# Kernel tuning notes

Measured on AMD Instinct MI355X. Metric: run time of the kernel, lower is better.

## Reference

```python
import jax, jax.numpy as jnp
import numpy as np

BS, Q, NC, T = 8, 500, 2, 400


def setup_inputs() -> dict:
    key = jax.random.key(0)
    k1, k2, k3, k4, k5 = jax.random.split(key, 5)
    pred_logits = jax.random.normal(k1, (BS, Q, NC), dtype=jnp.float32)
    pred_keypoints = jax.random.normal(k2, (BS, Q, 53), dtype=jnp.float32)
    tgt_ids = jax.random.randint(k3, (T,), 0, NC)
    # target keypoints: [center(2) | offsets(34)] ~ N(0, .2), visibility(17) in {0,1}
    tgt_xy = 0.2 * jax.random.normal(k4, (T, 36), dtype=jnp.float32)
    tgt_vis = jax.random.randint(k5, (T, 17), 0, 2).astype(jnp.float32)
    tgt_keypoints = jnp.concatenate([tgt_xy, tgt_vis], axis=1)
    return {"pred_logits": pred_logits, "pred_keypoints": pred_keypoints,
            "tgt_ids": tgt_ids, "tgt_keypoints": tgt_keypoints, "num_boxes": T}


def reference(pred_logits, pred_keypoints, tgt_ids, tgt_keypoints, num_boxes):
    """Fused batched cost-matrix construction of HungarianMatcher.forward.
    Returns C of shape [bs, num_queries, total_targets] (the matrix handed to
    scipy linear_sum_assignment in the original)."""
    cost_class_w, l_deltas, l_vis, l_ctr, l_abs = 1.0, 0.5, 0.2, 0.5, 4.0
    bs, q, nc = pred_logits.shape
    nb = jnp.asarray(num_boxes, jnp.float32)

    out_prob = jax.nn.softmax(pred_logits.reshape(-1, nc), axis=-1)   # [N, NC]
    kp = pred_keypoints.reshape(-1, 53)                               # [N, 53]
    C_pred, Z_pred, V_pred = kp[:, :2], kp[:, 2:36], kp[:, 36:]
    C_gt, Z_gt, V_gt = tgt_keypoints[:, :2], tgt_keypoints[:, 2:36], tgt_keypoints[:, 36:]

    t = tgt_keypoints.shape[0]
    # absolute keypoint positions: tile center per keypoint then add offsets
    A_gt = jnp.tile(C_gt[:, None, :], (1, 17, 1)).reshape(t, 34) + Z_gt       # [T, 34]
    A_pred = jnp.tile(C_pred[:, None, :], (1, 17, 1)).reshape(-1, 34) + Z_pred  # [N, 34]

    cost_class = -out_prob[:, tgt_ids]                                # [N, T]
    Vgt_ = jnp.repeat(V_gt, 2, axis=1)                                # [T, 34]

    # visibility-masked L1 distances (fuses the per-target cdist loop)
    offset_loss = jnp.sum(jnp.abs((Z_pred[:, None, :] - Z_gt[None, :, :]) * Vgt_[None, :, :]), axis=-1) / nb
    abs_loss = jnp.sum(jnp.abs((A_pred[:, None, :] - A_gt[None, :, :]) * Vgt_[None, :, :]), axis=-1) / nb
    # squared-L2 distances
    viz_loss = jnp.sum((V_pred[:, None, :] - V_gt[None, :, :]) ** 2, axis=-1) / nb
    center_loss = jnp.sum((C_pred[:, None, :] - C_gt[None, :, :]) ** 2, axis=-1) / nb

    C = (cost_class_w * cost_class + l_deltas * offset_loss + l_vis * viz_loss
         + l_ctr * center_loss + l_abs * abs_loss)
    return C.reshape(bs, q, t)
```

## Files before the change

kernel.cpp:

```cpp
#include <hip/hip_runtime.h>

#define P_TOT 4000
#define T_TOT 400
#define PP    8

__global__ __launch_bounds__(256) void hm_cost_kernel(
    const float* __restrict__ logits,
    const float* __restrict__ kp,
    const int*   __restrict__ tgt_ids,
    const float* __restrict__ tk,
    const int*   __restrict__ num_boxes,
    float*       __restrict__ out)
{
    const int t     = blockIdx.x * blockDim.x + threadIdx.x;
    const bool valid = (t < T_TOT);
    const int tc    = valid ? t : (T_TOT - 1);

    const float nbinv = 1.0f / (float)(*num_boxes);

    const float* trow = tk + tc * 53;
    const float Cg0 = trow[0];
    const float Cg1 = trow[1];
    float Zg[34];
#pragma unroll
    for (int k = 0; k < 34; ++k) Zg[k] = trow[2 + k];
    float Vg[17];
#pragma unroll
    for (int j = 0; j < 17; ++j) Vg[j] = trow[36 + j];
    const int cls = tgt_ids[tc];

    const int pbase = blockIdx.y * PP;

#pragma unroll 1
    for (int pi = 0; pi < PP; ++pi) {
        const int p = pbase + pi;
        const float* prow = kp + p * 53;

        const float l0 = logits[p * 2 + 0];
        const float l1 = logits[p * 2 + 1];
        const float m  = fmaxf(l0, l1);
        const float e0 = __expf(l0 - m);
        const float e1 = __expf(l1 - m);
        const float sinv = 1.0f / (e0 + e1);
        const float prob = (cls == 0 ? e0 : e1) * sinv;

        const float dc0 = prow[0] - Cg0;
        const float dc1 = prow[1] - Cg1;

        float off = 0.f, ab = 0.f;
#pragma unroll
        for (int j = 0; j < 17; ++j) {
            const float v   = Vg[j];
            const float dz0 = prow[2 + 2 * j]     - Zg[2 * j];
            const float dz1 = prow[2 + 2 * j + 1] - Zg[2 * j + 1];
            off += (fabsf(dz0) + fabsf(dz1)) * v;
            ab  += (fabsf(dz0 + dc0) + fabsf(dz1 + dc1)) * v;
        }

        float viz = 0.f;
#pragma unroll
        for (int j = 0; j < 17; ++j) {
            const float d = prow[36 + j] - Vg[j];
            viz += d * d;
        }

        const float ctr = dc0 * dc0 + dc1 * dc1;

        const float c = -prob
                      + (0.5f * off + 4.0f * ab + 0.2f * viz + 0.5f * ctr) * nbinv;

        if (valid) out[p * T_TOT + t] = c;
    }
}

extern "C" void kernel_launch(void* const* d_in, const int* in_sizes, int n_in,
                              void* d_out, int out_size, void* d_ws, size_t ws_size,
                              hipStream_t stream) {
    const float* logits    = (const float*)d_in[0];
    const float* kp        = (const float*)d_in[1];
    const int*   tgt_ids   = (const int*)  d_in[2];
    const float* tk        = (const float*)d_in[3];
    const int*   num_boxes = (const int*)  d_in[4];
    float*       out       = (float*)d_out;

    dim3 grid((T_TOT + 255) / 256, P_TOT / PP);
    hm_cost_kernel<<<grid, 256, 0, stream>>>(logits, kp, tgt_ids, tk, num_boxes, out);
}
```

Measured before the change: 83.28 us.

## Use one 448-thread block per prediction group and expand the squared-distance algebra

Replaces the 2D grid of 256-thread blocks, which left half the threads of the second block idle, with a 1D grid where one 448-thread block covers all 400 targets. This cuts wasted lanes and halves the number of times each prediction row is loaded. The visibility squared distance is expanded as sum(vp^2) - 2*vp·vg + sum(vg^2), with sum(vg^2) hoisted per target. The two-class softmax is simplified to a single exp. The expanded form can lose a little floating-point accuracy through cancellation.

```diff
diff --git a/kernel.cpp b/kernel.cpp
--- a/kernel.cpp
+++ b/kernel.cpp
@@ -3,8 +3,9 @@
 #define P_TOT 4000
 #define T_TOT 400
 #define PP    8
+#define BD    448
 
-__global__ __launch_bounds__(256) void hm_cost_kernel(
+__global__ __launch_bounds__(BD, 3) void hm_cost_kernel(
     const float* __restrict__ logits,
     const float* __restrict__ kp,
     const int*   __restrict__ tgt_ids,
@@ -12,9 +13,9 @@
     const int*   __restrict__ num_boxes,
     float*       __restrict__ out)
 {
-    const int t     = blockIdx.x * blockDim.x + threadIdx.x;
+    const int t      = threadIdx.x;
     const bool valid = (t < T_TOT);
-    const int tc    = valid ? t : (T_TOT - 1);
+    const int tc     = valid ? t : (T_TOT - 1);
 
     const float nbinv = 1.0f / (float)(*num_boxes);
 
@@ -25,45 +26,46 @@
 #pragma unroll
     for (int k = 0; k < 34; ++k) Zg[k] = trow[2 + k];
     float Vg[17];
+    float sVg = 0.f;
 #pragma unroll
-    for (int j = 0; j < 17; ++j) Vg[j] = trow[36 + j];
-    const int cls = tgt_ids[tc];
+    for (int j = 0; j < 17; ++j) {
+        Vg[j] = trow[36 + j];
+        sVg += Vg[j] * Vg[j];
+    }
+    const bool cls1 = (tgt_ids[tc] != 0);
 
-    const int pbase = blockIdx.y * PP;
+    const int pbase = blockIdx.x * PP;
 
 #pragma unroll 1
     for (int pi = 0; pi < PP; ++pi) {
         const int p = pbase + pi;
         const float* prow = kp + p * 53;
 
-        const float l0 = logits[p * 2 + 0];
-        const float l1 = logits[p * 2 + 1];
-        const float m  = fmaxf(l0, l1);
-        const float e0 = __expf(l0 - m);
-        const float e1 = __expf(l1 - m);
-        const float sinv = 1.0f / (e0 + e1);
-        const float prob = (cls == 0 ? e0 : e1) * sinv;
+        const float l0 = logits[2 * p];
+        const float l1 = logits[2 * p + 1];
+        const float q  = __expf(l1 - l0);
+        const float p0 = 1.0f / (1.0f + q);
+        const float prob = cls1 ? (q * p0) : p0;
 
         const float dc0 = prow[0] - Cg0;
         const float dc1 = prow[1] - Cg1;
 
-        float off = 0.f, ab = 0.f;
+        float off = 0.f, ab = 0.f, vv = 0.f, sVp = 0.f;
 #pragma unroll
         for (int j = 0; j < 17; ++j) {
             const float v   = Vg[j];
-            const float dz0 = prow[2 + 2 * j]     - Zg[2 * j];
-            const float dz1 = prow[2 + 2 * j + 1] - Zg[2 * j + 1];
+            const float zp0 = prow[2 + 2 * j];
+            const float zp1 = prow[3 + 2 * j];
+            const float dz0 = zp0 - Zg[2 * j];
+            const float dz1 = zp1 - Zg[2 * j + 1];
             off += (fabsf(dz0) + fabsf(dz1)) * v;
             ab  += (fabsf(dz0 + dc0) + fabsf(dz1 + dc1)) * v;
+            const float vp = prow[36 + j];
+            vv  += vp * v;
+            sVp += vp * vp;
         }
 
-        float viz = 0.f;
-#pragma unroll
-        for (int j = 0; j < 17; ++j) {
-            const float d = prow[36 + j] - Vg[j];
-            viz += d * d;
-        }
-
+        const float viz = sVp - 2.f * vv + sVg;
         const float ctr = dc0 * dc0 + dc1 * dc1;
 
         const float c = -prob
@@ -83,6 +85,6 @@
     const int*   num_boxes = (const int*)  d_in[4];
     float*       out       = (float*)d_out;
 
-    dim3 grid((T_TOT + 255) / 256, P_TOT / PP);
-    hm_cost_kernel<<<grid, 256, 0, stream>>>(logits, kp, tgt_ids, tk, num_boxes, out);
+    hm_cost_kernel<<<P_TOT / PP, BD, 0, stream>>>(logits, kp, tgt_ids, tk,
+                                                  num_boxes, out);
 }
```

Measured after the change: 78.12 us. 6.2% less time.
